# Performance work log

Measured on AMD Instinct MI355X. Metric: run time of the kernel, lower is better.

## Reference

```python
import jax, jax.numpy as jnp
import numpy as np

NUM_HEADS = 16
LAMBDA = 0.1
HADAMARD_SCALE = 0.05
ROPE_BASE = 10000.0


def _rope(t):
    # t: [B, H, S, hd] -- rotary embedding (half-split convention)
    hd = t.shape[-1]
    S = t.shape[2]
    half = hd // 2
    inv_freq = 1.0 / (ROPE_BASE ** (jnp.arange(half, dtype=jnp.float32) / half))
    ang = jnp.arange(S, dtype=jnp.float32)[:, None] * inv_freq[None, :]  # [S, half]
    cos = jnp.cos(ang).astype(t.dtype)
    sin = jnp.sin(ang).astype(t.dtype)
    t1, t2 = t[..., :half], t[..., half:]
    return jnp.concatenate([t1 * cos - t2 * sin, t2 * cos + t1 * sin], axis=-1)


def _rotate_half(t):
    half = t.shape[-1] // 2
    return jnp.concatenate([-t[..., half:], t[..., :half]], axis=-1)


def setup_inputs() -> dict:
    key = jax.random.key(0)
    ks = jax.random.split(key, 6)
    B, S, D = 2, 2048, 1024
    scale = 1.0 / np.sqrt(D).astype(np.float32)
    x = jax.random.normal(ks[0], (B, S, D), jnp.float32)
    Wq = jax.random.normal(ks[1], (D, D), jnp.float32) * scale
    Wk = jax.random.normal(ks[2], (D, D), jnp.float32) * scale
    Wv = jax.random.normal(ks[3], (D, D), jnp.float32) * scale
    Wo = jax.random.normal(ks[4], (D, D), jnp.float32) * scale
    gate_w = jax.random.normal(ks[5], (D // NUM_HEADS,), jnp.float32) * 0.01
    return {"x": x, "Wq": Wq, "Wk": Wk, "Wv": Wv, "Wo": Wo, "gate_w": gate_w}


def reference(x, Wq, Wk, Wv, Wo, gate_w):
    B, S, D = x.shape
    H = NUM_HEADS
    hd = D // H

    def heads(W):
        return (x @ W.T).reshape(B, S, H, hd).transpose(0, 2, 1, 3)  # [B,H,S,hd]

    Q = _rope(heads(Wq))
    K = _rope(heads(Wk))
    V = heads(Wv)

    causal = jnp.tril(jnp.ones((S, S), dtype=bool))
    inv_sqrt_d = 1.0 / jnp.sqrt(jnp.asarray(hd, x.dtype))

    def attend(q, k):
        # first-order + lambda * second-order (elementwise-squared) scores
        s = (jnp.einsum('bhsd,bhtd->bhst', q, k)
             + LAMBDA * jnp.einsum('bhsd,bhtd->bhst', q * q, k * k)) * inv_sqrt_d
        s = jnp.where(causal, s, jnp.asarray(-1e9, s.dtype))
        a = jax.nn.softmax(s, axis=-1)
        return jnp.einsum('bhst,bhtd->bhsd', a, V)

    out1 = attend(Q, K)                                  # standard pass
    out2 = attend(_rotate_half(Q), _rotate_half(K))      # rotated second pass

    # hadamard gate mix of the two passes
    out = 0.5 * (out1 + out2) + HADAMARD_SCALE * (out1 * out2) * gate_w

    out = out.transpose(0, 2, 1, 3).reshape(B, S, D)
    return out @ Wo.T
```

## Files before the change

### kernel.cpp

```cpp
#include <hip/hip_runtime.h>

typedef unsigned short u16;
typedef __attribute__((ext_vector_type(4))) unsigned short u16x4;
typedef __attribute__((ext_vector_type(8))) unsigned short u16x8;
typedef __attribute__((ext_vector_type(8))) short s16x8;
typedef __attribute__((ext_vector_type(4))) float f32x4;

__device__ __forceinline__ u16 f2bf(float f) {
  unsigned int u = __float_as_uint(f);
  u += 0x7FFFu + ((u >> 16) & 1u);
  return (u16)(u >> 16);
}
__device__ __forceinline__ float bf2f(u16 h) {
  return __uint_as_float(((unsigned int)h) << 16);
}

__device__ __forceinline__ void gload_lds16(const u16* g, u16* l) {
  __builtin_amdgcn_global_load_lds(
      (const __attribute__((address_space(1))) unsigned int*)(g),
      (__attribute__((address_space(3))) unsigned int*)(l), 16, 0, 0);
}

__global__ __launch_bounds__(256) void cvt_kernel(const float* __restrict__ src,
                                                  u16* __restrict__ dst, int n4) {
  int i = blockIdx.x * 256 + threadIdx.x;
  if (i >= n4) return;
  float4 v = reinterpret_cast<const float4*>(src)[i];
  u16x4 o;
  o.x = f2bf(v.x); o.y = f2bf(v.y); o.z = f2bf(v.z); o.w = f2bf(v.w);
  reinterpret_cast<u16x4*>(dst)[i] = o;
}

__global__ __launch_bounds__(256) void cvt_w(const float* __restrict__ Wq,
                                             const float* __restrict__ Wk,
                                             const float* __restrict__ Wv,
                                             const float* __restrict__ Wo,
                                             u16* __restrict__ wbf, u16* __restrict__ wobf) {
  int blk = blockIdx.x;
  int sel = blk >> 10;
  const float* src = (sel == 0) ? Wq : (sel == 1) ? Wk : (sel == 2) ? Wv : Wo;
  u16* dst = (sel < 3) ? (wbf + (size_t)sel * 1048576) : wobf;
  int i = (blk & 1023) * 256 + threadIdx.x;
  float4 v = reinterpret_cast<const float4*>(src)[i];
  u16x4 o;
  o.x = f2bf(v.x); o.y = f2bf(v.y); o.z = f2bf(v.z); o.w = f2bf(v.w);
  reinterpret_cast<u16x4*>(dst)[i] = o;
}

__device__ __forceinline__ void store_out(float* p, float v) { *p = v; }
__device__ __forceinline__ void store_out(u16* p, float v) { *p = f2bf(v); }

template <typename OutT>
__global__ __launch_bounds__(256) void gemm_bt(const u16* __restrict__ A,
                                               const u16* __restrict__ Bw,
                                               OutT* __restrict__ C, int N, int K) {
  __shared__ u16 As[4096];
  __shared__ u16 Bs[4096];
  const int tid = threadIdx.x;
  const int lane = tid & 63;
  const int wave = tid >> 6;
  const int wm = wave >> 1, wn = wave & 1;
  const int lh = lane & 15, quad = lane >> 4;
  const int q8 = quad * 8;
  const int m0 = blockIdx.y * 128, n0 = blockIdx.x * 128;

  f32x4 acc[4][4];
#pragma unroll
  for (int i = 0; i < 4; ++i)
#pragma unroll
    for (int j = 0; j < 4; ++j) { acc[i][j][0] = 0.f; acc[i][j][1] = 0.f; acc[i][j][2] = 0.f; acc[i][j][3] = 0.f; }

  const int nkt = K >> 5;
  for (int kt = 0; kt < nkt; ++kt) {
    const int kb = kt * 32;
    __syncthreads();
#pragma unroll
    for (int i = 0; i < 4; ++i) {
      const int c = wave * 4 + i;
      if (c < 8) {
        gload_lds16(A + (size_t)(m0 + c * 16 + lh) * K + kb + q8, &As[c * 512 + lane * 8]);
      } else {
        const int rb = c - 8;
        gload_lds16(Bw + (size_t)(n0 + rb * 16 + lh) * K + kb + q8, &Bs[rb * 512 + lane * 8]);
      }
    }
    __syncthreads();
    s16x8 af[4], bf4[4];
#pragma unroll
    for (int mb = 0; mb < 4; ++mb)
      af[mb] = *reinterpret_cast<const s16x8*>(&As[(wm * 4 + mb) * 512 + lane * 8]);
#pragma unroll
    for (int nb = 0; nb < 4; ++nb)
      bf4[nb] = *reinterpret_cast<const s16x8*>(&Bs[(wn * 4 + nb) * 512 + lane * 8]);
#pragma unroll
    for (int mb = 0; mb < 4; ++mb)
#pragma unroll
      for (int nb = 0; nb < 4; ++nb)
        acc[mb][nb] = __builtin_amdgcn_mfma_f32_16x16x32_bf16(af[mb], bf4[nb], acc[mb][nb], 0, 0, 0);
  }
#pragma unroll
  for (int mb = 0; mb < 4; ++mb)
#pragma unroll
    for (int nb = 0; nb < 4; ++nb) {
      const int col = n0 + wn * 64 + nb * 16 + lh;
#pragma unroll
      for (int r = 0; r < 4; ++r) {
        const int row = m0 + wm * 64 + mb * 16 + quad * 4 + r;
        store_out(&C[(size_t)row * N + col], acc[mb][nb][r]);
      }
    }
}

__global__ __launch_bounds__(256) void rope_kernel(const u16* __restrict__ raw,
                                                   u16* __restrict__ Qs, u16* __restrict__ Q2s,
                                                   u16* __restrict__ Kb, u16* __restrict__ K2b) {
  int idx = blockIdx.x * 256 + threadIdx.x;
  int which = idx >> 21;
  int id = idx & 0x1FFFFF;
  int d = id & 31;
  int s = (id >> 5) & 2047;
  int bh = id >> 16;
  int b = bh >> 4;
  int h = bh & 15;
  const u16* r = raw + (size_t)(b * 2048 + s) * 3072 + which * 1024 + h * 64 + d;
  float v1 = bf2f(r[0]);
  float v2 = bf2f(r[32]);
  float invf = __expf((float)d * -0.2878231366f);
  float ang = (float)s * invf;
  float sv, cv;
  __sincosf(ang, &sv, &cv);
  float e0 = v1 * cv - v2 * sv;
  float e1 = v2 * cv + v1 * sv;
  size_t ofs = (size_t)(bh * 2048 + s) * 64 + d;
  if (which == 0) {
    Qs[ofs]       = f2bf(e0 * 0.125f);
    Qs[ofs + 32]  = f2bf(e1 * 0.125f);
    Q2s[ofs]      = f2bf(e0 * e0 * 0.0125f);
    Q2s[ofs + 32] = f2bf(e1 * e1 * 0.0125f);
  } else {
    Kb[ofs]       = f2bf(e0);
    Kb[ofs + 32]  = f2bf(e1);
    K2b[ofs]      = f2bf(e0 * e0);
    K2b[ofs + 32] = f2bf(e1 * e1);
  }
}

__global__ __launch_bounds__(256) void transpose_v(const u16* __restrict__ raw,
                                                   u16* __restrict__ Vt) {
  int st = blockIdx.x, bh = blockIdx.y;
  int b = bh >> 4, h = bh & 15;
  __shared__ u16 tile[64 * 72];
  int tid = threadIdx.x;
#pragma unroll
  for (int it = 0; it < 4; ++it) {
    int c = it * 256 + tid;
    int sr = c >> 4, d4 = c & 15;
    u16x4 v = *reinterpret_cast<const u16x4*>(
        raw + (size_t)(b * 2048 + st * 64 + sr) * 3072 + 2048 + h * 64 + d4 * 4);
    *reinterpret_cast<u16x4*>(&tile[sr * 72 + d4 * 4]) = v;
  }
  __syncthreads();
#pragma unroll
  for (int it = 0; it < 4; ++it) {
    int c = it * 256 + tid;
    int dd = c >> 4, s4 = c & 15;
    u16x4 v;
#pragma unroll
    for (int j = 0; j < 4; ++j) v[j] = tile[(s4 * 4 + j) * 72 + dd];
    *reinterpret_cast<u16x4*>(Vt + (size_t)(bh * 64 + dd) * 2048 + st * 64 + s4 * 4) = v;
  }
}

__global__ __launch_bounds__(256, 2) void attn_kernel(const u16* __restrict__ Qs,
                                                      const u16* __restrict__ Q2s,
                                                      const u16* __restrict__ Kb,
                                                      const u16* __restrict__ K2b,
                                                      const u16* __restrict__ Vt,
                                                      const float* __restrict__ gate,
                                                      u16* __restrict__ attn) {
  const int qi = 15 - (int)blockIdx.x;
  const int bh = blockIdx.y;
  const int tid = threadIdx.x, lane = tid & 63, wave = tid >> 6;
  const int lh = lane & 15, quad = lane >> 4;
  const int b = bh >> 4, h = bh & 15;
  __shared__ u16 stageS[2][8192];
  __shared__ u16 Pbuf[4][2][1152];
  const int base = qi * 128 + wave * 32;
  const int q8 = quad * 8;

  auto do_stage = [&](int buf, int kt) {
#pragma unroll
    for (int i = 0; i < 4; ++i) {
      const int c = wave * 4 + i;
      const int t = c >> 3, f = c & 7, kk = f >> 2, nb = f & 3;
      const u16* src = (t ? K2b : Kb) +
          (size_t)(bh * 2048 + kt * 64 + nb * 16 + lh) * 64 + kk * 32 + q8;
      gload_lds16(src, &stageS[buf][t * 4096 + f * 512 + lane * 8]);
    }
  };

  s16x8 qf[2][2], q2f[2][2];
#pragma unroll
  for (int mb = 0; mb < 2; ++mb) {
    const size_t qoff = (size_t)(bh * 2048 + base + mb * 16 + lh) * 64 + q8;
#pragma unroll
    for (int kk = 0; kk < 2; ++kk) {
      qf[mb][kk]  = *reinterpret_cast<const s16x8*>(Qs + qoff + kk * 32);
      q2f[mb][kk] = *reinterpret_cast<const s16x8*>(Q2s + qoff + kk * 32);
    }
  }

  f32x4 oacc[2][4];
  float lsum[2][4];
#pragma unroll
  for (int mb = 0; mb < 2; ++mb)
#pragma unroll
    for (int nb = 0; nb < 4; ++nb) { oacc[mb][nb][0] = 0.f; oacc[mb][nb][1] = 0.f; oacc[mb][nb][2] = 0.f; oacc[mb][nb][3] = 0.f; }
#pragma unroll
  for (int mb = 0; mb < 2; ++mb)
#pragma unroll
    for (int r = 0; r < 4; ++r) lsum[mb][r] = 0.f;
  float gw[4];
#pragma unroll
  for (int nb = 0; nb < 4; ++nb) gw[nb] = gate[nb * 16 + lh];

  do_stage(0, 0);
  __syncthreads();

  const int ktmax = 2 * qi + 1;
  const int wmaxrow = base + 31;
  for (int kt = 0; kt <= ktmax; ++kt) {
    const int p = kt & 1;
    if (kt < ktmax) do_stage(1 - p, kt + 1);

    if (kt * 64 <= wmaxrow) {
      const u16* Ks = stageS[p];
      f32x4 sacc[2][4];
#pragma unroll
      for (int mb = 0; mb < 2; ++mb)
#pragma unroll
        for (int nb = 0; nb < 4; ++nb) { sacc[mb][nb][0] = -8.f; sacc[mb][nb][1] = -8.f; sacc[mb][nb][2] = -8.f; sacc[mb][nb][3] = -8.f; }
#pragma unroll
      for (int nb = 0; nb < 4; ++nb)
#pragma unroll
        for (int kk = 0; kk < 2; ++kk) {
          s16x8 kf  = *reinterpret_cast<const s16x8*>(&Ks[(kk * 4 + nb) * 512 + lane * 8]);
          s16x8 k2f = *reinterpret_cast<const s16x8*>(&Ks[4096 + (kk * 4 + nb) * 512 + lane * 8]);
#pragma unroll
          for (int mb = 0; mb < 2; ++mb) {
            sacc[mb][nb] = __builtin_amdgcn_mfma_f32_16x16x32_bf16(qf[mb][kk],  kf,  sacc[mb][nb], 0, 0, 0);
            sacc[mb][nb] = __builtin_amdgcn_mfma_f32_16x16x32_bf16(q2f[mb][kk], k2f, sacc[mb][nb], 0, 0, 0);
          }
        }
      s16x8 vf[2][4];
#pragma unroll
      for (int kk = 0; kk < 2; ++kk)
#pragma unroll
        for (int nb = 0; nb < 4; ++nb)
          vf[kk][nb] = *reinterpret_cast<const s16x8*>(
              Vt + (size_t)(bh * 64 + nb * 16 + lh) * 2048 + kt * 64 + kk * 32 + q8);

      if (kt * 64 + 63 > base) {
#pragma unroll
        for (int mb = 0; mb < 2; ++mb)
#pragma unroll
          for (int nb = 0; nb < 4; ++nb) {
            const int colg = kt * 64 + nb * 16 + lh;
#pragma unroll
            for (int r = 0; r < 4; ++r) {
              const int rowg = base + mb * 16 + quad * 4 + r;
              if (colg > rowg) sacc[mb][nb][r] = -1e9f;
            }
          }
      }
#pragma unroll
      for (int mb = 0; mb < 2; ++mb)
#pragma unroll
        for (int nb = 0; nb < 4; ++nb)
#pragma unroll
          for (int r = 0; r < 4; ++r) {
            float pv = __expf(sacc[mb][nb][r]);
            lsum[mb][r] += pv;
            Pbuf[wave][mb][(quad * 4 + r) * 72 + nb * 16 + lh] = f2bf(pv);
          }
#pragma unroll
      for (int mb = 0; mb < 2; ++mb)
#pragma unroll
        for (int kk = 0; kk < 2; ++kk) {
          s16x8 pf = *reinterpret_cast<const s16x8*>(&Pbuf[wave][mb][lh * 72 + kk * 32 + q8]);
#pragma unroll
          for (int nb = 0; nb < 4; ++nb)
            oacc[mb][nb] = __builtin_amdgcn_mfma_f32_16x16x32_bf16(pf, vf[kk][nb], oacc[mb][nb], 0, 0, 0);
        }
    }
    __syncthreads();
  }
#pragma unroll
  for (int mb = 0; mb < 2; ++mb)
#pragma unroll
    for (int r = 0; r < 4; ++r) {
      float rs = lsum[mb][r];
#pragma unroll
      for (int off = 1; off < 16; off <<= 1) rs += __shfl_xor(rs, off);
      lsum[mb][r] = 1.0f / rs;
    }
#pragma unroll
  for (int mb = 0; mb < 2; ++mb)
#pragma unroll
    for (int nb = 0; nb < 4; ++nb)
#pragma unroll
      for (int r = 0; r < 4; ++r) {
        float o = oacc[mb][nb][r] * lsum[mb][r];
        float val = o + 0.05f * o * o * gw[nb];
        const int rows = base + mb * 16 + quad * 4 + r;
        attn[(size_t)(b * 2048 + rows) * 1024 + h * 64 + nb * 16 + lh] = f2bf(val);
      }
}

extern "C" void kernel_launch(void* const* d_in, const int* in_sizes, int n_in,
                              void* d_out, int out_size, void* d_ws, size_t ws_size,
                              hipStream_t stream) {
  (void)in_sizes; (void)n_in; (void)out_size; (void)ws_size;
  const float* x    = (const float*)d_in[0];
  const float* Wq   = (const float*)d_in[1];
  const float* Wk   = (const float*)d_in[2];
  const float* Wv   = (const float*)d_in[3];
  const float* Wo   = (const float*)d_in[4];
  const float* gate = (const float*)d_in[5];

  u16* ws    = (u16*)d_ws;
  u16* xbf   = ws;
  u16* wbf   = xbf + 4194304;
  u16* wobf  = wbf + 3145728;
  u16* raw   = wobf + 1048576;
  u16* Qsb   = raw + 12582912;
  u16* Kbb   = Qsb + 4194304;
  u16* K2bb  = Kbb + 4194304;
  u16* Vtb   = K2bb + 4194304;
  u16* Q2sb  = xbf;
  u16* attnb = raw;

  cvt_kernel<<<4096, 256, 0, stream>>>(x, xbf, 1048576);
  cvt_w<<<4096, 256, 0, stream>>>(Wq, Wk, Wv, Wo, wbf, wobf);

  gemm_bt<u16><<<dim3(24, 32), 256, 0, stream>>>(xbf, wbf, raw, 3072, 1024);
  rope_kernel<<<16384, 256, 0, stream>>>(raw, Qsb, Q2sb, Kbb, K2bb);
  transpose_v<<<dim3(32, 32), 256, 0, stream>>>(raw, Vtb);
  attn_kernel<<<dim3(16, 32), 256, 0, stream>>>(Qsb, Q2sb, Kbb, K2bb, Vtb, gate, attnb);
  gemm_bt<float><<<dim3(8, 32), 256, 0, stream>>>(attnb, wobf, (float*)d_out, 1024, 1024);
}
```

Measured before the change: 274.0 us.

## Split long causal attention rows across two blocks with a combine pass

Query tiles in the upper half of the sequence have their key range split into two halves, each handled by a separate block that writes unnormalized partial outputs and row sums to fp32 workspace. A new combine kernel adds the partials, normalizes, applies the gate mix and writes bf16. The grid grows from 16 to 24 blocks per head, aiming to balance the causal triangle workload and raise occupancy. The cost is an extra kernel launch and fp32 partial traffic. The code relies on the softmax needing no running max, since scores are offset by a fixed constant.

```diff
diff --git a/kernel.cpp b/kernel.cpp
--- a/kernel.cpp
+++ b/kernel.cpp
@@ -177,8 +177,15 @@
                                                       const u16* __restrict__ K2b,
                                                       const u16* __restrict__ Vt,
                                                       const float* __restrict__ gate,
-                                                      u16* __restrict__ attn) {
-  const int qi = 15 - (int)blockIdx.x;
+                                                      u16* __restrict__ attn,
+                                                      float* __restrict__ Opart,
+                                                      float* __restrict__ Lpart) {
+  const int bx = blockIdx.x;
+  const int g = bx / 3, t = bx - 3 * g;
+  int qi, kt0, kt1, half;
+  bool split;
+  if (t < 2) { qi = 15 - g; split = true;  half = t; const int nk = qi + 1; kt0 = t * nk; kt1 = kt0 + nk - 1; }
+  else       { qi = 7 - g;  split = false; half = 0; kt0 = 0; kt1 = 2 * qi + 1; }
   const int bh = blockIdx.y;
   const int tid = threadIdx.x, lane = tid & 63, wave = tid >> 6;
   const int lh = lane & 15, quad = lane >> 4;
@@ -192,10 +199,10 @@
 #pragma unroll
     for (int i = 0; i < 4; ++i) {
       const int c = wave * 4 + i;
-      const int t = c >> 3, f = c & 7, kk = f >> 2, nb = f & 3;
-      const u16* src = (t ? K2b : Kb) +
+      const int t2 = c >> 3, f = c & 7, kk = f >> 2, nb = f & 3;
+      const u16* src = (t2 ? K2b : Kb) +
           (size_t)(bh * 2048 + kt * 64 + nb * 16 + lh) * 64 + kk * 32 + q8;
-      gload_lds16(src, &stageS[buf][t * 4096 + f * 512 + lane * 8]);
+      gload_lds16(src, &stageS[buf][t2 * 4096 + f * 512 + lane * 8]);
     }
   };
 
@@ -224,14 +231,13 @@
 #pragma unroll
   for (int nb = 0; nb < 4; ++nb) gw[nb] = gate[nb * 16 + lh];
 
-  do_stage(0, 0);
+  do_stage(0, kt0);
   __syncthreads();
 
-  const int ktmax = 2 * qi + 1;
   const int wmaxrow = base + 31;
-  for (int kt = 0; kt <= ktmax; ++kt) {
-    const int p = kt & 1;
-    if (kt < ktmax) do_stage(1 - p, kt + 1);
+  for (int kt = kt0; kt <= kt1; ++kt) {
+    const int p = (kt - kt0) & 1;
+    if (kt < kt1) do_stage(1 - p, kt + 1);
 
     if (kt * 64 <= wmaxrow) {
       const u16* Ks = stageS[p];
@@ -302,19 +308,52 @@
       float rs = lsum[mb][r];
 #pragma unroll
       for (int off = 1; off < 16; off <<= 1) rs += __shfl_xor(rs, off);
-      lsum[mb][r] = 1.0f / rs;
-    }
-#pragma unroll
-  for (int mb = 0; mb < 2; ++mb)
-#pragma unroll
-    for (int nb = 0; nb < 4; ++nb)
+      lsum[mb][r] = rs;
+    }
+  if (split) {
+#pragma unroll
+    for (int mb = 0; mb < 2; ++mb)
 #pragma unroll
       for (int r = 0; r < 4; ++r) {
-        float o = oacc[mb][nb][r] * lsum[mb][r];
-        float val = o + 0.05f * o * o * gw[nb];
+        const int rowRel = base + mb * 16 + quad * 4 + r - 1024;
+        const size_t orow = ((size_t)half * 32768 + bh * 1024 + rowRel);
+        if (lh == 0) Lpart[orow] = lsum[mb][r];
+#pragma unroll
+        for (int nb = 0; nb < 4; ++nb)
+          Opart[orow * 64 + nb * 16 + lh] = oacc[mb][nb][r];
+      }
+  } else {
+#pragma unroll
+    for (int mb = 0; mb < 2; ++mb)
+#pragma unroll
+      for (int r = 0; r < 4; ++r) {
+        const float invl = 1.0f / lsum[mb][r];
         const int rows = base + mb * 16 + quad * 4 + r;
-        attn[(size_t)(b * 2048 + rows) * 1024 + h * 64 + nb * 16 + lh] = f2bf(val);
-      }
+#pragma unroll
+        for (int nb = 0; nb < 4; ++nb) {
+          float o = oacc[mb][nb][r] * invl;
+          float val = o + 0.05f * o * o * gw[nb];
+          attn[(size_t)(b * 2048 + rows) * 1024 + h * 64 + nb * 16 + lh] = f2bf(val);
+        }
+      }
+  }
+}
+
+__global__ __launch_bounds__(256) void combine_kernel(const float* __restrict__ Opart,
+                                                      const float* __restrict__ Lpart,
+                                                      const float* __restrict__ gate,
+                                                      u16* __restrict__ attn) {
+  int idx = blockIdx.x * 256 + threadIdx.x;
+  int d = idx & 63;
+  int rowi = idx >> 6;
+  int bh = rowi >> 10, rr = rowi & 1023;
+  float o = Opart[idx] + Opart[idx + 2097152];
+  float l = Lpart[rowi] + Lpart[rowi + 32768];
+  o /= l;
+  float val = o + 0.05f * o * o * gate[d];
+  int b = bh >> 4, h = bh & 15;
+  int s = 1024 + rr;
+  attn[(size_t)(b * 2048 + s) * 1024 + h * 64 + d] = f2bf(val);
 }
 
 extern "C" void kernel_launch(void* const* d_in, const int* in_sizes, int n_in,
@@ -337,6 +376,8 @@
   u16* Kbb   = Qsb + 4194304;
   u16* K2bb  = Kbb + 4194304;
   u16* Vtb   = K2bb + 4194304;
+  float* Opart = (float*)(Vtb + 4194304);
+  float* Lpart = Opart + 4194304;
   u16* Q2sb  = xbf;
   u16* attnb = raw;
 
@@ -346,6 +387,8 @@
   gemm_bt<u16><<<dim3(24, 32), 256, 0, stream>>>(xbf, wbf, raw, 3072, 1024);
   rope_kernel<<<16384, 256, 0, stream>>>(raw, Qsb, Q2sb, Kbb, K2bb);
   transpose_v<<<dim3(32, 32), 256, 0, stream>>>(raw, Vtb);
-  attn_kernel<<<dim3(16, 32), 256, 0, stream>>>(Qsb, Q2sb, Kbb, K2bb, Vtb, gate, attnb);
+  attn_kernel<<<dim3(24, 32), 256, 0, stream>>>(Qsb, Q2sb, Kbb, K2bb, Vtb, gate, attnb,
+                                                Opart, Lpart);
+  combine_kernel<<<8192, 256, 0, stream>>>(Opart, Lpart, gate, attnb);
   gemm_bt<float><<<dim3(8, 32), 256, 0, stream>>>(attnb, wobf, (float*)d_out, 1024, 1024);
 }
```

After: 268.3 us. -2.1%, faster.
